# Kernel tuning notes

Hardware: AMD Instinct MI355X
Metric: run time of the kernel (lower is better)

Reference implementation:

```python
import jax, jax.numpy as jnp
import numpy as np

PATCH = 8
TOP_K = 512
EPS = 1e-8


def setup_inputs() -> dict:
    key = jax.random.key(0)
    # uniform [0,1): keeps max+min > 0 so the contrast ratio is well-behaved,
    # matching pixel-intensity inputs the module expects.
    images = jax.random.uniform(key, (64, 3, 512, 512), dtype=jnp.float32)
    return {"images": images}


def _divide_in_patches(images):
    # [B,C,H,W] -> [B, nH*nW, C, p, p]
    B, C, H, W = images.shape
    nh, nw = H // PATCH, W // PATCH
    p = images.reshape(B, C, nh, PATCH, nw, PATCH)
    p = p.transpose(0, 2, 4, 1, 3, 5)
    return p.reshape(B, nh * nw, C, PATCH, PATCH)


def reference(images):
    patches = _divide_in_patches(images)          # [B,P,C,p,p]
    B, P = patches.shape[0], patches.shape[1]
    # contrast heuristic: max/min over channels and patch pixels
    mx = patches.max(axis=(2, 3, 4))              # [B,P]
    mn = patches.min(axis=(2, 3, 4))              # [B,P]
    contrast = (mx - mn + EPS) / (mx + mn)        # [B,P]
    # deterministic top-k per image (probabilistic=False branch)
    _, idx = jax.lax.top_k(contrast, TOP_K)       # [B,K] int32
    mask = jnp.zeros((B, P), dtype=patches.dtype)
    mask = mask.at[jnp.arange(B)[:, None], idx].set(1.0)
    return patches * mask[:, :, None, None, None]  # masked patches
```

## Files before the change

kernel.cpp:

```cpp
#include <hip/hip_runtime.h>
#include <hip/hip_bf16.h>


#define B_IMG 64
#define NPAT 4096
#define TOPK 512

typedef float f32x4 __attribute__((ext_vector_type(4)));

#define KEY_BITS 42

__device__ __forceinline__ unsigned long long make_key(unsigned int fb, int p) {
    return ((unsigned long long)fb << 12) | (unsigned)(NPAT - 1 - p);
}

__global__ __launch_bounds__(256) void contrast_kernel(const float* __restrict__ in,
                                                       float* __restrict__ contrast) {
    const int blk = blockIdx.x;
    const int b  = blk >> 6;
    const int ph = blk & 63;
    const int tid = threadIdx.x;
    const int pw  = tid >> 2;
    const int sub = tid & 3;

    float mx = -1e30f, mn = 1e30f;
    #pragma unroll
    for (int i = 0; i < 6; ++i) {
        const int r  = sub * 6 + i;
        const int c  = r >> 3;
        const int py = r & 7;
        const size_t base = (((size_t)b * 3 + c) * 512 + (size_t)ph * 8 + py) * 512
                          + (size_t)pw * 8;
        const float4* rp = (const float4*)(in + base);
        float4 a = rp[0];
        float4 d = rp[1];
        mx = fmaxf(mx, fmaxf(fmaxf(a.x, a.y), fmaxf(a.z, a.w)));
        mx = fmaxf(mx, fmaxf(fmaxf(d.x, d.y), fmaxf(d.z, d.w)));
        mn = fminf(mn, fminf(fminf(a.x, a.y), fminf(a.z, a.w)));
        mn = fminf(mn, fminf(fminf(d.x, d.y), fminf(d.z, d.w)));
    }
    mx = fmaxf(mx, __shfl_xor(mx, 1));
    mx = fmaxf(mx, __shfl_xor(mx, 2));
    mn = fminf(mn, __shfl_xor(mn, 1));
    mn = fminf(mn, __shfl_xor(mn, 2));

    if (sub == 0) {
        const float ctr = (mx - mn + 1e-8f) / (mx + mn);
        contrast[(size_t)b * NPAT + (size_t)ph * 64 + pw] = ctr;
    }
}

__global__ __launch_bounds__(256) void topk_kernel(const float* __restrict__ contrast,
                                                   unsigned long long* __restrict__ thresh) {
    const int b   = blockIdx.x;
    const int tid = threadIdx.x;
    const float4* row4 = (const float4*)(contrast + (size_t)b * NPAT);

    unsigned long long k[16];
    #pragma unroll
    for (int j = 0; j < 4; ++j) {
        const float4 v = row4[tid * 4 + j];
        const int base = tid * 16 + j * 4;
        k[j * 4 + 0] = make_key(__float_as_uint(v.x), base + 0);
        k[j * 4 + 1] = make_key(__float_as_uint(v.y), base + 1);
        k[j * 4 + 2] = make_key(__float_as_uint(v.z), base + 2);
        k[j * 4 + 3] = make_key(__float_as_uint(v.w), base + 3);
    }

    __shared__ int wsum[4];
    unsigned long long lo = 0ULL;
    unsigned long long hi = 1ULL << KEY_BITS;

    for (int it = 0; it < KEY_BITS; ++it) {
        const unsigned long long mid = (lo + hi) >> 1;
        int c = 0;
        #pragma unroll
        for (int j = 0; j < 16; ++j) c += (k[j] >= mid) ? 1 : 0;
        #pragma unroll
        for (int off = 32; off > 0; off >>= 1) c += __shfl_xor(c, off);
        if ((tid & 63) == 0) wsum[tid >> 6] = c;
        __syncthreads();
        const int total = wsum[0] + wsum[1] + wsum[2] + wsum[3];
        if (total >= TOPK) lo = mid; else hi = mid;
        __syncthreads();
    }
    if (tid == 0) thresh[b] = lo;
}

__global__ __launch_bounds__(256) void write_kernel(const float* __restrict__ in,
                                                    const float* __restrict__ contrast,
                                                    const unsigned long long* __restrict__ thresh,
                                                    f32x4* __restrict__ out) {
    const int blk = blockIdx.x;
    const int b  = blk >> 6;
    const int ph = blk & 63;

    __shared__ int sel[64];
    if (threadIdx.x < 64) {
        const int p = ph * 64 + threadIdx.x;
        const unsigned int fb = __float_as_uint(contrast[(size_t)b * NPAT + p]);
        sel[threadIdx.x] = (make_key(fb, p) >= thresh[b]) ? 1 : 0;
    }
    __syncthreads();

    const f32x4* in4 = (const f32x4*)in;
    const size_t out_base = ((size_t)b * NPAT + (size_t)ph * 64) * 48;

    #pragma unroll
    for (int it = 0; it < 12; ++it) {
        const int idx = it * 256 + threadIdx.x;
        const int pl  = idx / 48;
        const int rem = idx - pl * 48;
        f32x4 v = (f32x4){0.f, 0.f, 0.f, 0.f};
        if (sel[pl]) {
            const int c    = rem >> 4;
            const int t    = rem & 15;
            const int py   = t >> 1;
            const int half = t & 1;
            const size_t a = (((size_t)b * 3 + c) * 512 + (size_t)ph * 8 + py) * 128
                           + (size_t)pl * 2 + half;
            v = in4[a];
        }
        __builtin_nontemporal_store(v, &out[out_base + idx]);
    }
}

extern "C" void kernel_launch(void* const* d_in, const int* in_sizes, int n_in,
                              void* d_out, int out_size, void* d_ws, size_t ws_size,
                              hipStream_t stream) {
    const float* in = (const float*)d_in[0];
    float* out = (float*)d_out;

    float* contrast = (float*)d_ws;
    unsigned long long* thresh =
        (unsigned long long*)((char*)d_ws + (size_t)B_IMG * NPAT * sizeof(float));

    contrast_kernel<<<B_IMG * 64, 256, 0, stream>>>(in, contrast);
    topk_kernel<<<B_IMG, 256, 0, stream>>>(contrast, thresh);
    write_kernel<<<B_IMG * 64, 256, 0, stream>>>(in, contrast, thresh, (f32x4*)out);
}
```

Measured before the change: 355.5 us.

## Zero output during contrast pass and gather only top-k selected patches

The output zeroing moves into the contrast kernel, with alternate blocks doing zero stores, so the final kernel only reads and writes the 512 selected patches per image instead of every patch. The top-k kernel now narrows its bisection range to the actual key min/max, uses double-buffered shared partial sums to drop one barrier per iteration, and emits an explicit index list through a shared atomic counter. Total memory traffic drops because unselected patches are no longer read in the final pass. In exchange, the selected patches are written twice (zero, then data), and the gather writes are scattered.

New measurement: 373.7 us. +5.1%, slower.

```diff
diff --git a/kernel.cpp b/kernel.cpp
--- a/kernel.cpp
+++ b/kernel.cpp
@@ -1,5 +1,4 @@
 #include <hip/hip_runtime.h>
-#include <hip/hip_bf16.h>
 
 
 #define B_IMG 64
@@ -8,25 +7,44 @@
 
 typedef float f32x4 __attribute__((ext_vector_type(4)));
 
-#define KEY_BITS 42
-
 __device__ __forceinline__ unsigned long long make_key(unsigned int fb, int p) {
     return ((unsigned long long)fb << 12) | (unsigned)(NPAT - 1 - p);
 }
 
-__global__ __launch_bounds__(256) void contrast_kernel(const float* __restrict__ in,
-                                                       float* __restrict__ contrast) {
-    const int blk = blockIdx.x;
-    const int b  = blk >> 6;
-    const int ph = blk & 63;
-    const int tid = threadIdx.x;
-    const int pw  = tid >> 2;
-    const int sub = tid & 3;
+__device__ __forceinline__ unsigned long long shfl_xor_u64(unsigned long long v, int m) {
+    unsigned int lo = (unsigned int)v;
+    unsigned int hi = (unsigned int)(v >> 32);
+    lo = __shfl_xor(lo, m);
+    hi = __shfl_xor(hi, m);
+    return ((unsigned long long)hi << 32) | lo;
+}
+
+__global__ __launch_bounds__(256) void contrast_zero_kernel(const float* __restrict__ in,
+                                                            float* __restrict__ contrast,
+                                                            f32x4* __restrict__ out) {
+    const int blk  = blockIdx.x;
+    const int role = blk & 1;
+    const int sub  = blk >> 1;
+    const int tid  = threadIdx.x;
+
+    if (role) {
+        const size_t base = (size_t)sub * 3072;
+        const f32x4 z = (f32x4){0.f, 0.f, 0.f, 0.f};
+        #pragma unroll
+        for (int it = 0; it < 12; ++it)
+            __builtin_nontemporal_store(z, &out[base + (size_t)it * 256 + tid]);
+        return;
+    }
+
+    const int b  = sub >> 6;
+    const int ph = sub & 63;
+    const int pw = tid >> 2;
+    const int s4 = tid & 3;
 
     float mx = -1e30f, mn = 1e30f;
     #pragma unroll
     for (int i = 0; i < 6; ++i) {
-        const int r  = sub * 6 + i;
+        const int r  = s4 * 6 + i;
         const int c  = r >> 3;
         const int py = r & 7;
         const size_t base = (((size_t)b * 3 + c) * 512 + (size_t)ph * 8 + py) * 512
@@ -44,14 +62,14 @@
     mn = fminf(mn, __shfl_xor(mn, 1));
     mn = fminf(mn, __shfl_xor(mn, 2));
 
-    if (sub == 0) {
+    if (s4 == 0) {
         const float ctr = (mx - mn + 1e-8f) / (mx + mn);
         contrast[(size_t)b * NPAT + (size_t)ph * 64 + pw] = ctr;
     }
 }
 
 __global__ __launch_bounds__(256) void topk_kernel(const float* __restrict__ contrast,
-                                                   unsigned long long* __restrict__ thresh) {
+                                                   int* __restrict__ list) {
     const int b   = blockIdx.x;
     const int tid = threadIdx.x;
     const float4* row4 = (const float4*)(contrast + (size_t)b * NPAT);
@@ -67,61 +85,88 @@
         k[j * 4 + 3] = make_key(__float_as_uint(v.w), base + 3);
     }
 
-    __shared__ int wsum[4];
-    unsigned long long lo = 0ULL;
-    unsigned long long hi = 1ULL << KEY_BITS;
+    unsigned long long mn = k[0], mx = k[0];
+    #pragma unroll
+    for (int j = 1; j < 16; ++j) {
+        mn = (k[j] < mn) ? k[j] : mn;
+        mx = (k[j] > mx) ? k[j] : mx;
+    }
+    #pragma unroll
+    for (int off = 32; off > 0; off >>= 1) {
+        unsigned long long on = shfl_xor_u64(mn, off);
+        unsigned long long ox = shfl_xor_u64(mx, off);
+        mn = (on < mn) ? on : mn;
+        mx = (ox > mx) ? ox : mx;
+    }
+    __shared__ unsigned long long smm[8];
+    if ((tid & 63) == 0) { smm[tid >> 6] = mn; smm[4 + (tid >> 6)] = mx; }
+    __syncthreads();
+    unsigned long long lo = smm[0];
+    unsigned long long hi = smm[4];
+    #pragma unroll
+    for (int w = 1; w < 4; ++w) {
+        lo = (smm[w] < lo) ? smm[w] : lo;
+        hi = (smm[4 + w] > hi) ? smm[4 + w] : hi;
+    }
 
-    for (int it = 0; it < KEY_BITS; ++it) {
-        const unsigned long long mid = (lo + hi) >> 1;
+    __shared__ int wsum[2][4];
+    int parity = 0;
+    while (hi - lo > 1ULL) {
+        const unsigned long long mid = lo + ((hi - lo) >> 1);
         int c = 0;
         #pragma unroll
         for (int j = 0; j < 16; ++j) c += (k[j] >= mid) ? 1 : 0;
         #pragma unroll
         for (int off = 32; off > 0; off >>= 1) c += __shfl_xor(c, off);
-        if ((tid & 63) == 0) wsum[tid >> 6] = c;
+        if ((tid & 63) == 0) wsum[parity][tid >> 6] = c;
         __syncthreads();
-        const int total = wsum[0] + wsum[1] + wsum[2] + wsum[3];
+        const int total = wsum[parity][0] + wsum[parity][1]
+                        + wsum[parity][2] + wsum[parity][3];
         if (total >= TOPK) lo = mid; else hi = mid;
-        __syncthreads();
+        parity ^= 1;
     }
-    if (tid == 0) thresh[b] = lo;
+
+    __shared__ int cnt;
+    if (tid == 0) cnt = 0;
+    __syncthreads();
+    int* mylist = list + b * TOPK;
+    #pragma unroll
+    for (int j = 0; j < 16; ++j) {
+        if (k[j] >= lo) {
+            const int pos = atomicAdd(&cnt, 1);
+            mylist[pos] = tid * 16 + j;
+        }
+    }
 }
 
-__global__ __launch_bounds__(256) void write_kernel(const float* __restrict__ in,
-                                                    const float* __restrict__ contrast,
-                                                    const unsigned long long* __restrict__ thresh,
-                                                    f32x4* __restrict__ out) {
-    const int blk = blockIdx.x;
-    const int b  = blk >> 6;
-    const int ph = blk & 63;
+__global__ __launch_bounds__(256) void gather_kernel(const float* __restrict__ in,
+                                                     const int* __restrict__ list,
+                                                     f32x4* __restrict__ out) {
+    const int blk   = blockIdx.x;
+    const int b     = blk >> 5;
+    const int chunk = blk & 31;
+    const int tid   = threadIdx.x;
 
-    __shared__ int sel[64];
-    if (threadIdx.x < 64) {
-        const int p = ph * 64 + threadIdx.x;
-        const unsigned int fb = __float_as_uint(contrast[(size_t)b * NPAT + p]);
-        sel[threadIdx.x] = (make_key(fb, p) >= thresh[b]) ? 1 : 0;
-    }
+    __shared__ int plist[16];
+    if (tid < 16) plist[tid] = list[b * TOPK + chunk * 16 + tid];
     __syncthreads();
 
     const f32x4* in4 = (const f32x4*)in;
-    const size_t out_base = ((size_t)b * NPAT + (size_t)ph * 64) * 48;
-
     #pragma unroll
-    for (int it = 0; it < 12; ++it) {
-        const int idx = it * 256 + threadIdx.x;
+    for (int it = 0; it < 3; ++it) {
+        const int idx = it * 256 + tid;
         const int pl  = idx / 48;
         const int rem = idx - pl * 48;
-        f32x4 v = (f32x4){0.f, 0.f, 0.f, 0.f};
-        if (sel[pl]) {
-            const int c    = rem >> 4;
-            const int t    = rem & 15;
-            const int py   = t >> 1;
-            const int half = t & 1;
-            const size_t a = (((size_t)b * 3 + c) * 512 + (size_t)ph * 8 + py) * 128
-                           + (size_t)pl * 2 + half;
-            v = in4[a];
-        }
-        __builtin_nontemporal_store(v, &out[out_base + idx]);
+        const int p   = plist[pl];
+        const int c    = rem >> 4;
+        const int t    = rem & 15;
+        const int py   = t >> 1;
+        const int half = t & 1;
+        const int ph = p >> 6, pw = p & 63;
+        const size_t a = (((size_t)b * 3 + c) * 512 + (size_t)ph * 8 + py) * 128
+                       + (size_t)pw * 2 + half;
+        const f32x4 v = in4[a];
+        __builtin_nontemporal_store(v, &out[((size_t)b * NPAT + p) * 48 + rem]);
     }
 }
 
@@ -129,13 +174,12 @@
                               void* d_out, int out_size, void* d_ws, size_t ws_size,
                               hipStream_t stream) {
     const float* in = (const float*)d_in[0];
-    float* out = (float*)d_out;
+    f32x4* out = (f32x4*)d_out;
 
     float* contrast = (float*)d_ws;
-    unsigned long long* thresh =
-        (unsigned long long*)((char*)d_ws + (size_t)B_IMG * NPAT * sizeof(float));
+    int* list = (int*)((char*)d_ws + (size_t)B_IMG * NPAT * sizeof(float));
 
-    contrast_kernel<<<B_IMG * 64, 256, 0, stream>>>(in, contrast);
-    topk_kernel<<<B_IMG, 256, 0, stream>>>(contrast, thresh);
-    write_kernel<<<B_IMG * 64, 256, 0, stream>>>(in, contrast, thresh, (f32x4*)out);
+    contrast_zero_kernel<<<2 * B_IMG * 64, 256, 0, stream>>>(in, contrast, out);
+    topk_kernel<<<B_IMG, 256, 0, stream>>>(contrast, list);
+    gather_kernel<<<B_IMG * 32, 256, 0, stream>>>(in, list, out);
 }
```
